# Kernel tuning notes

Measured on AMD Instinct MI355X. Metric: run time of the kernel, lower is better.

Reference implementation:

```python
import jax, jax.numpy as jnp
import numpy as np

D_MODEL = 768
NUM_HEADS = 12
DEPTH = D_MODEL // NUM_HEADS


def setup_inputs() -> dict:
    key = jax.random.key(0)
    ks = jax.random.split(key, 11)
    B, S = 2, 2048
    s = 1.0 / np.sqrt(D_MODEL)
    inp = {
        "Q": jax.random.normal(ks[0], (B, S, D_MODEL), jnp.float32),
        "K": jax.random.normal(ks[1], (B, S, D_MODEL), jnp.float32),
        "V": jax.random.normal(ks[2], (B, S, D_MODEL), jnp.float32),
        "Wq": jax.random.normal(ks[3], (D_MODEL, D_MODEL), jnp.float32) * s,
        "bq": jnp.zeros((D_MODEL,), jnp.float32),
        "Wk": jax.random.normal(ks[4], (D_MODEL, D_MODEL), jnp.float32) * s,
        "bk": jnp.zeros((D_MODEL,), jnp.float32),
        "Wv": jax.random.normal(ks[5], (D_MODEL, D_MODEL), jnp.float32) * s,
        "bv": jnp.zeros((D_MODEL,), jnp.float32),
        "Wo": jax.random.normal(ks[6], (D_MODEL, D_MODEL), jnp.float32) * s,
        "bo": jnp.zeros((D_MODEL,), jnp.float32),
    }
    return inp


def _split_heads(x):
    B, S, _ = x.shape
    return x.reshape(B, S, NUM_HEADS, DEPTH).transpose(0, 2, 1, 3)  # [B,H,S,d]


def reference(Q, K, V, Wq, bq, Wk, bk, Wv, bv, Wo, bo):
    q = _split_heads(Q @ Wq.T + bq)  # [B,H,S,d]
    k = _split_heads(K @ Wk.T + bk)
    v = _split_heads(V @ Wv.T + bv)
    scale = 1.0 / jnp.sqrt(jnp.asarray(DEPTH, q.dtype))
    scores = jnp.einsum('bhqd,bhkd->bhqk', q, k) * scale  # [B,H,S,S]
    weights = jax.nn.softmax(scores, axis=-1)
    attn = jnp.einsum('bhqk,bhkd->bhqd', weights, v)  # [B,H,S,d]
    B, H, S, d = attn.shape
    attn = attn.transpose(0, 2, 1, 3).reshape(B, S, H * d)
    out = attn @ Wo.T + bo
    return (out, weights)
```

## Files before the change

### kernel.cpp

```cpp
#include <hip/hip_runtime.h>
#include <hip/hip_bf16.h>

typedef __attribute__((ext_vector_type(4)))  float f32x4;
typedef __attribute__((ext_vector_type(16))) float f32x16;
typedef __attribute__((ext_vector_type(8)))  short s16x8;

#define MFMA(a,b,c)   __builtin_amdgcn_mfma_f32_16x16x32_bf16(a,b,c,0,0,0)
#define MFMA32(a,b,c) __builtin_amdgcn_mfma_f32_32x32x16_bf16(a,b,c,0,0,0)

__device__ __forceinline__ void gll16(const void* gptr, void* lptr){
  auto g = (const __attribute__((address_space(1))) unsigned int*)gptr;
  auto l = (__attribute__((address_space(3))) unsigned int*)lptr;
  __builtin_amdgcn_global_load_lds(g, l, 16, 0, 0);
}

__device__ __forceinline__ void split2(float x, __hip_bfloat16& h, __hip_bfloat16& l){
  h = __float2bfloat16(x);
  l = __float2bfloat16(x - __bfloat162float(h));
}

__device__ __forceinline__ unsigned short bf16bits(float x){
  __hip_bfloat16 h = __float2bfloat16(x);
  return *reinterpret_cast<unsigned short*>(&h);
}
__device__ __forceinline__ unsigned pack2(float lo, float hi){
  return (unsigned)bf16bits(lo) | ((unsigned)bf16bits(hi) << 16);
}
__device__ __forceinline__ void plane32swap(unsigned &a, unsigned &b){
  asm volatile("v_permlane32_swap_b32 %0, %1" : "+v"(a), "+v"(b));
}

__global__ __launch_bounds__(256) void split_all(
  const float* __restrict__ Q, const float* __restrict__ K, const float* __restrict__ V,
  const float* __restrict__ Wq, const float* __restrict__ Wk,
  const float* __restrict__ Wv, const float* __restrict__ Wo,
  __hip_bfloat16* __restrict__ QIh,
  __hip_bfloat16* __restrict__ KIh,
  __hip_bfloat16* __restrict__ VIh,
  __hip_bfloat16* __restrict__ Wqh,
  __hip_bfloat16* __restrict__ Wkh,
  __hip_bfloat16* __restrict__ Wvh,
  __hip_bfloat16* __restrict__ Woh, __hip_bfloat16* __restrict__ Wol)
{
  const int NE4 = 786432, WE4 = 147456;
  int i = blockIdx.x*256 + threadIdx.x;
  const float* src; __hip_bfloat16 *dh, *dl = nullptr; int off;
  if (i < 3*NE4){
    int seg = i / NE4; off = i - seg*NE4;
    src = seg==0 ? Q   : (seg==1 ? K   : V);
    dh  = seg==0 ? QIh : (seg==1 ? KIh : VIh);
  } else {
    int j = i - 3*NE4; int seg = j / WE4; off = j - seg*WE4;
    src = seg==0 ? Wq  : (seg==1 ? Wk  : (seg==2 ? Wv  : Wo));
    dh  = seg==0 ? Wqh : (seg==1 ? Wkh : (seg==2 ? Wvh : Woh));
    if (seg == 3) dl = Wol;
  }
  float4 x = ((const float4*)src)[off];
  __hip_bfloat16 h0,l0,h1,l1,h2,l2,h3,l3;
  split2(x.x,h0,l0); split2(x.y,h1,l1); split2(x.z,h2,l2); split2(x.w,h3,l3);
  union { __hip_bfloat16 b[4]; ushort4 u; } H, L;
  H.b[0]=h0; H.b[1]=h1; H.b[2]=h2; H.b[3]=h3;
  L.b[0]=l0; L.b[1]=l1; L.b[2]=l2; L.b[3]=l3;
  *(ushort4*)(dh + (size_t)off*4) = H.u;
  if (dl) *(ushort4*)(dl + (size_t)off*4) = L.u;
}

__global__ __launch_bounds__(256) void gemm_qkv(
    const __hip_bfloat16* __restrict__ QAh,
    const __hip_bfloat16* __restrict__ KAh,
    const __hip_bfloat16* __restrict__ VAh,
    const __hip_bfloat16* __restrict__ WqH,
    const __hip_bfloat16* __restrict__ WkH,
    const __hip_bfloat16* __restrict__ WvH,
    const float* __restrict__ bq, const float* __restrict__ bk, const float* __restrict__ bv,
    float qscale,
    __hip_bfloat16* __restrict__ qhp, __hip_bfloat16* __restrict__ qlp,
    __hip_bfloat16* __restrict__ khp, __hip_bfloat16* __restrict__ vTp)
{
  __shared__ __align__(16) __hip_bfloat16 lds[16384];

  const int tid = threadIdx.x;
  const int w = tid >> 6, lane = tid & 63, r = lane & 15, g = lane >> 4;
  const int wg = blockIdx.x;
  const int seg = wg / 768;
  const int t = wg % 768;
  const int tm = t / 12, tn = t % 12;

  const __hip_bfloat16* Ah = seg==0 ? QAh : (seg==1 ? KAh : VAh);
  const __hip_bfloat16* Bh = seg==0 ? WqH : (seg==1 ? WkH : WvH);
  const float* bias        = seg==0 ? bq  : (seg==1 ? bk  : bv);

  const char* gA_h = (const char*)Ah + (size_t)tm*64*768*2;
  const char* gB_h = (const char*)Bh + (size_t)tn*64*768*2;

  f32x4 acc[4] = {};

  auto stage = [&](int buf, int kbe){
    #pragma unroll
    for (int i = 0; i < 2; ++i){
      int lb = i*4096 + tid*16;
      int row = lb >> 7, colb = lb & 127;
      gll16(gA_h + (size_t)row*1536 + kbe*2 + colb, (char*)lds + buf*16384 + i*4096 + w*1024);
      gll16(gB_h + (size_t)row*1536 + kbe*2 + colb, (char*)lds + buf*16384 + 8192 + i*4096 + w*1024);
    }
  };
  int cur = 0;
  stage(0, 0);
  __syncthreads();
  for (int it = 0; it < 12; ++it){
    if (it + 1 < 12) stage(cur ^ 1, (it+1)*64);
    const __hip_bfloat16* A = lds + cur*8192;
    const __hip_bfloat16* B = lds + cur*8192 + 4096;
    #pragma unroll
    for (int c = 0; c < 2; ++c){
      int aoff = (w*16 + r)*64 + c*32 + g*8;
      s16x8 a_h = *(const s16x8*)(A + aoff);
      #pragma unroll
      for (int j = 0; j < 4; ++j){
        s16x8 b_h = *(const s16x8*)(B + (j*16 + r)*64 + c*32 + g*8);
        acc[j] = MFMA(a_h, b_h, acc[j]);
      }
    }
    __syncthreads();
    cur ^= 1;
  }

  #pragma unroll
  for (int j = 0; j < 4; ++j){
    #pragma unroll
    for (int e = 0; e < 4; ++e){
      int m = tm*64 + w*16 + g*4 + e;
      int n = tn*64 + j*16 + r;
      float v = acc[j][e] + bias[n];
      int b = m >> 11, s = m & 2047;
      if (seg == 0){
        v *= qscale;
        __hip_bfloat16 h, l; split2(v, h, l);
        size_t idx = ((size_t)(b*12 + (n>>6))*2048 + s)*64 + (n & 63);
        qhp[idx] = h; qlp[idx] = l;
      } else if (seg == 1){
        size_t idx = ((size_t)(b*12 + (n>>6))*2048 + s)*64 + (n & 63);
        khp[idx] = __float2bfloat16(v);
      } else {
        size_t idx = ((size_t)(b*12 + (n>>6))*64 + (n & 63))*2048 + s;
        vTp[idx] = __float2bfloat16(v);
      }
    }
  }
}

__global__ __launch_bounds__(256) void gemm_o(
    const __hip_bfloat16* __restrict__ Ah, const __hip_bfloat16* __restrict__ Al,
    const __hip_bfloat16* __restrict__ Bh, const __hip_bfloat16* __restrict__ Bl,
    const float* __restrict__ bias, float* __restrict__ o_f)
{
  __shared__ __align__(16) __hip_bfloat16 sAh[64*64];
  __shared__ __align__(16) __hip_bfloat16 sAl[64*64];
  __shared__ __align__(16) __hip_bfloat16 sBh[64*64];
  __shared__ __align__(16) __hip_bfloat16 sBl[64*64];

  const int tid = threadIdx.x;
  const int w = tid >> 6, lane = tid & 63, r = lane & 15, g = lane >> 4;
  const int t = blockIdx.x;
  const int tm = t / 12, tn = t % 12;

  const char* gA_h = (const char*)Ah + (size_t)tm*64*768*2;
  const char* gA_l = (const char*)Al + (size_t)tm*64*768*2;
  const char* gB_h = (const char*)Bh + (size_t)tn*64*768*2;
  const char* gB_l = (const char*)Bl + (size_t)tn*64*768*2;

  f32x4 acc[4] = {};

  for (int kb = 0; kb < 768; kb += 64){
    __syncthreads();
    #pragma unroll
    for (int i = 0; i < 2; ++i){
      int lb = i*4096 + tid*16;
      int row = lb >> 7, colb = lb & 127;
      gll16(gA_h + (size_t)row*1536 + kb*2 + colb, (char*)sAh + i*4096 + w*1024);
      gll16(gA_l + (size_t)row*1536 + kb*2 + colb, (char*)sAl + i*4096 + w*1024);
      gll16(gB_h + (size_t)row*1536 + kb*2 + colb, (char*)sBh + i*4096 + w*1024);
      gll16(gB_l + (size_t)row*1536 + kb*2 + colb, (char*)sBl + i*4096 + w*1024);
    }
    __syncthreads();
    #pragma unroll
    for (int c = 0; c < 2; ++c){
      int aoff = (w*16 + r)*64 + c*32 + g*8;
      s16x8 a_h = *(const s16x8*)(sAh + aoff);
      s16x8 a_l = *(const s16x8*)(sAl + aoff);
      #pragma unroll
      for (int j = 0; j < 4; ++j){
        int boff = (j*16 + r)*64 + c*32 + g*8;
        s16x8 b_h = *(const s16x8*)(sBh + boff);
        s16x8 b_l = *(const s16x8*)(sBl + boff);
        acc[j] = MFMA(a_h, b_h, acc[j]);
        acc[j] = MFMA(a_l, b_h, acc[j]);
        acc[j] = MFMA(a_h, b_l, acc[j]);
      }
    }
  }

  #pragma unroll
  for (int j = 0; j < 4; ++j){
    #pragma unroll
    for (int e = 0; e < 4; ++e){
      int m = tm*64 + w*16 + g*4 + e;
      int n = tn*64 + j*16 + r;
      o_f[(size_t)m*768 + n] = acc[j][e] + bias[n];
    }
  }
}

__global__ __launch_bounds__(256,4) void attn_l(
    const __hip_bfloat16* __restrict__ qh,
    const __hip_bfloat16* __restrict__ kh,
    float* __restrict__ rlbuf)
{
  __shared__ float ldsL[128];
  const int tid  = threadIdx.x;
  const int w    = tid >> 6;
  const int lane = tid & 63;
  const int col  = lane & 31;
  const int hi   = lane >> 5;
  const int bh = blockIdx.x % 24, qt = blockIdx.x / 24;

  const __hip_bfloat16* qr_h = qh + ((size_t)bh*2048 + qt*32 + col)*64 + hi*8;
  s16x8 Qh[4];
  #pragma unroll
  for (int ks = 0; ks < 4; ++ks) Qh[ks] = *(const s16x8*)(qr_h + ks*16);

  const __hip_bfloat16* kb = kh + (size_t)bh*2048*64;

  s16x8 kfn[4];
  {
    const __hip_bfloat16* kr = kb + ((size_t)(w*16)*32 + col)*64 + hi*8;
    #pragma unroll
    for (int ks = 0; ks < 4; ++ks) kfn[ks] = *(const s16x8*)(kr + ks*16);
  }

  float ps0=0.f, ps1=0.f, ps2=0.f, ps3=0.f;
  for (int c = 0; c < 16; ++c){
    s16x8 kf[4];
    #pragma unroll
    for (int ks = 0; ks < 4; ++ks) kf[ks] = kfn[ks];
    if (c < 15){
      const __hip_bfloat16* kr = kb + ((size_t)(w*16 + c + 1)*32 + col)*64 + hi*8;
      #pragma unroll
      for (int ks = 0; ks < 4; ++ks) kfn[ks] = *(const s16x8*)(kr + ks*16);
    }
    f32x16 s0;
    #pragma unroll
    for (int e = 0; e < 16; ++e) s0[e] = 0.f;
    #pragma unroll
    for (int ks = 0; ks < 4; ++ks) s0 = MFMA32(kf[ks], Qh[ks], s0);
    #pragma unroll
    for (int e = 0; e < 16; e += 4){
      ps0 += exp2f(s0[e+0]); ps1 += exp2f(s0[e+1]);
      ps2 += exp2f(s0[e+2]); ps3 += exp2f(s0[e+3]);
    }
  }
  float l_w = (ps0+ps1) + (ps2+ps3);
  l_w += __shfl_xor(l_w, 32);
  if (lane < 32) ldsL[w*32 + col] = l_w;
  __syncthreads();
  if (tid < 32){
    float lt = (ldsL[tid] + ldsL[32+tid]) + (ldsL[64+tid] + ldsL[96+tid]);
    rlbuf[(size_t)bh*2048 + qt*32 + tid] = 1.0f / lt;
  }
}

__global__ __launch_bounds__(256,4) void attn_pv(
    const __hip_bfloat16* __restrict__ qh, const __hip_bfloat16* __restrict__ ql,
    const __hip_bfloat16* __restrict__ kh,
    const __hip_bfloat16* __restrict__ vT,
    const float* __restrict__ rlbuf,
    float* __restrict__ wout,
    __hip_bfloat16* __restrict__ attnh, __hip_bfloat16* __restrict__ attnl)
{
  __shared__ __align__(16) float ldsX[4*32*36];
  __shared__ float ldsRL[32];

  const int tid  = threadIdx.x;
  const int w    = tid >> 6;
  const int lane = tid & 63;
  const int col  = lane & 31;
  const int hi   = lane >> 5;
  const int bh = blockIdx.x % 24, qt = blockIdx.x / 24;

  const __hip_bfloat16* qr_h = qh + ((size_t)bh*2048 + qt*32 + col)*64 + hi*8;
  const __hip_bfloat16* qr_l = ql + ((size_t)bh*2048 + qt*32 + col)*64 + hi*8;
  s16x8 Qh[4], Ql[4];
  #pragma unroll
  for (int ks = 0; ks < 4; ++ks){
    Qh[ks] = *(const s16x8*)(qr_h + ks*16);
    Ql[ks] = *(const s16x8*)(qr_l + ks*16);
  }

  if (tid < 32) ldsRL[tid] = rlbuf[(size_t)bh*2048 + qt*32 + tid];
  __syncthreads();
  const float rl = ldsRL[col];

  const __hip_bfloat16* kb = kh + (size_t)bh*2048*64;
  const __hip_bfloat16* vb = vT + (size_t)bh*64*2048;
  float* W = ldsX + w*1152;

  s16x8 kfn[4];
  {
    const __hip_bfloat16* kr = kb + ((size_t)(w*16)*32 + col)*64 + hi*8;
    #pragma unroll
    for (int ks = 0; ks < 4; ++ks) kfn[ks] = *(const s16x8*)(kr + ks*16);
  }

  f32x16 pv0, pv1;
  #pragma unroll
  for (int e = 0; e < 16; ++e){ pv0[e]=0.f; pv1[e]=0.f; }
  float* wq = wout + ((size_t)bh*2048 + (size_t)qt*32)*2048;

  for (int c = 0; c < 16; ++c){
    const int key0 = (w*16 + c)*32;
    s16x8 kf[4];
    #pragma unroll
    for (int ks = 0; ks < 4; ++ks) kf[ks] = kfn[ks];
    if (c < 15){
      const __hip_bfloat16* kr = kb + ((size_t)(w*16 + c + 1)*32 + col)*64 + hi*8;
      #pragma unroll
      for (int ks = 0; ks < 4; ++ks) kfn[ks] = *(const s16x8*)(kr + ks*16);
    }
    s16x8 vv[2][2];
    #pragma unroll
    for (int ww = 0; ww < 2; ++ww)
      #pragma unroll
      for (int dt = 0; dt < 2; ++dt)
        vv[ww][dt] = *(const s16x8*)(vb + ((size_t)(dt*32+col)*2048 + key0 + ww*16 + hi*8));

    f32x16 s0;
    #pragma unroll
    for (int e = 0; e < 16; ++e) s0[e] = 0.f;
    #pragma unroll
    for (int ks = 0; ks < 4; ++ks){
      s0 = MFMA32(kf[ks], Qh[ks], s0);
      s0 = MFMA32(kf[ks], Ql[ks], s0);
    }
    #pragma unroll
    for (int e = 0; e < 16; ++e) s0[e] = exp2f(s0[e]);

    #pragma unroll
    for (int rq = 0; rq < 4; ++rq){
      f32x4 f;
      f[0]=s0[rq*4+0]*rl; f[1]=s0[rq*4+1]*rl; f[2]=s0[rq*4+2]*rl; f[3]=s0[rq*4+3]*rl;
      *(f32x4*)(W + col*36 + rq*8 + hi*4) = f;
    }
    #pragma unroll
    for (int it = 0; it < 4; ++it){
      int q  = it*8 + (lane>>3);
      int k4 = (lane&7)*4;
      f32x4 f = *(const f32x4*)(W + q*36 + k4);
      *(f32x4*)(wq + (size_t)q*2048 + key0 + k4) = f;
    }

    #pragma unroll
    for (int ww = 0; ww < 2; ++ww){
      const int e0 = ww*8;
      unsigned wa = pack2(s0[e0+0], s0[e0+1]);
      unsigned wb = pack2(s0[e0+2], s0[e0+3]);
      unsigned wc = pack2(s0[e0+4], s0[e0+5]);
      unsigned wd = pack2(s0[e0+6], s0[e0+7]);
      plane32swap(wa, wc);
      plane32swap(wb, wd);
      union { unsigned u[4]; s16x8 v; } cv;
      cv.u[0]=wa; cv.u[1]=wb; cv.u[2]=wc; cv.u[3]=wd;
      pv0 = MFMA32(cv.v, vv[ww][0], pv0);
      pv1 = MFMA32(cv.v, vv[ww][1], pv1);
    }
  }

  __syncthreads();

  float* ldsPV = ldsX;
  if (w >= 2){
    const int buf = w - 2;
    #pragma unroll
    for (int e = 0; e < 16; ++e){
      ldsPV[(e)   *128 + buf*64 + lane] = pv0[e];
      ldsPV[(16+e)*128 + buf*64 + lane] = pv1[e];
    }
  }
  __syncthreads();
  if (w < 2){
    #pragma unroll
    for (int e = 0; e < 16; ++e){
      pv0[e] += ldsPV[(e)   *128 + w*64 + lane];
      pv1[e] += ldsPV[(16+e)*128 + w*64 + lane];
    }
  }
  __syncthreads();
  if (w == 1){
    #pragma unroll
    for (int e = 0; e < 16; ++e){
      ldsPV[(e)   *128 + lane] = pv0[e];
      ldsPV[(16+e)*128 + lane] = pv1[e];
    }
  }
  __syncthreads();
  if (w == 0){
    #pragma unroll
    for (int e = 0; e < 16; ++e){
      pv0[e] += ldsPV[(e)   *128 + lane];
      pv1[e] += ldsPV[(16+e)*128 + lane];
    }
    const int b_ = bh / 12, hh = bh % 12;
    #pragma unroll
    for (int e = 0; e < 16; ++e){
      int qsub = (e&3) + 8*(e>>2) + 4*hi;
      float re = ldsRL[qsub];
      int qrow = qt*32 + qsub;
      size_t base = ((size_t)b_*2048 + qrow)*768 + hh*64;
      __hip_bfloat16 h0, l0, h1, l1;
      split2(pv0[e]*re, h0, l0);
      split2(pv1[e]*re, h1, l1);
      attnh[base + col]      = h0; attnl[base + col]      = l0;
      attnh[base + 32 + col] = h1; attnl[base + 32 + col] = l1;
    }
  }
}

extern "C" void kernel_launch(void* const* d_in, const int* in_sizes, int n_in,
                              void* d_out, int out_size, void* d_ws, size_t ws_size,
                              hipStream_t stream){
  const float* Q  = (const float*)d_in[0];
  const float* Kx = (const float*)d_in[1];
  const float* V  = (const float*)d_in[2];
  const float* Wq = (const float*)d_in[3];
  const float* bq = (const float*)d_in[4];
  const float* Wk = (const float*)d_in[5];
  const float* bk = (const float*)d_in[6];
  const float* Wv = (const float*)d_in[7];
  const float* bv = (const float*)d_in[8];
  const float* Wo = (const float*)d_in[9];
  const float* bo = (const float*)d_in[10];

  float* out = (float*)d_out;
  float* wts = out + (size_t)2*2048*768;

  char* cur = (char*)d_ws;
  auto alloc = [&](size_t elems)->__hip_bfloat16*{
    __hip_bfloat16* p = (__hip_bfloat16*)cur;
    cur += ((elems*2 + 255) & ~(size_t)255);
    return p;
  };
  const size_t NE = (size_t)4096*768;
  const size_t WE = (size_t)768*768;

  __hip_bfloat16 *QIh=alloc(NE), *KIh=alloc(NE), *VIh=alloc(NE);
  __hip_bfloat16 *Wqh=alloc(WE), *Wkh=alloc(WE), *Wvh=alloc(WE),
                 *Woh=alloc(WE), *Wol=alloc(WE);
  __hip_bfloat16 *qhp=alloc(NE), *qlp=alloc(NE), *khp=alloc(NE),
                 *vTp=alloc(NE);
  __hip_bfloat16 *ath=alloc(NE), *atl=alloc(NE);
  float* rlbuf = (float*)alloc(2*24*2048);

  split_all<<<11520, 256, 0, stream>>>(Q, Kx, V, Wq, Wk, Wv, Wo,
      QIh, KIh, VIh, Wqh, Wkh, Wvh, Woh, Wol);

  gemm_qkv<<<2304, 256, 0, stream>>>(
      QIh, KIh, VIh,
      Wqh, Wkh, Wvh,
      bq, bk, bv, 0.18033688011112042f,
      qhp, qlp, khp, vTp);

  attn_l <<<1536, 256, 0, stream>>>(qhp, khp, rlbuf);
  attn_pv<<<1536, 256, 0, stream>>>(qhp, qlp, khp, vTp, rlbuf, wts, ath, atl);

  gemm_o<<<768, 256, 0, stream>>>(ath,atl,Woh,Wol,bo, out);
}
```

Baseline: 273.1 us.

## Process two query tiles per attn_l block and prioritize MFMA waves

The row-sum kernel now handles 64 queries per block instead of 32, so each K fragment loaded is reused for two MFMA chains, which halves K loads and the grid size. Both attention kernels wrap their MFMA sections in s_setprio to raise wave priority during matrix work. In attn_pv the weights store through LDS to global is moved after the PV MFMAs, so the write traffic can overlap with later work. The cost is more registers in attn_l and fewer blocks to spread across CUs.

```diff
diff --git a/kernel.cpp b/kernel.cpp
--- a/kernel.cpp
+++ b/kernel.cpp
@@ -216,18 +216,22 @@
     const __hip_bfloat16* __restrict__ kh,
     float* __restrict__ rlbuf)
 {
-  __shared__ float ldsL[128];
+  __shared__ float ldsL[2][128];
   const int tid  = threadIdx.x;
   const int w    = tid >> 6;
   const int lane = tid & 63;
   const int col  = lane & 31;
   const int hi   = lane >> 5;
-  const int bh = blockIdx.x % 24, qt = blockIdx.x / 24;
-
-  const __hip_bfloat16* qr_h = qh + ((size_t)bh*2048 + qt*32 + col)*64 + hi*8;
-  s16x8 Qh[4];
+  const int bh = blockIdx.x % 24, qt2 = blockIdx.x / 24;
+
+  const __hip_bfloat16* qr0 = qh + ((size_t)bh*2048 + qt2*64 + col)*64 + hi*8;
+  const __hip_bfloat16* qr1 = qr0 + 32*64;
+  s16x8 Qh0[4], Qh1[4];
   #pragma unroll
-  for (int ks = 0; ks < 4; ++ks) Qh[ks] = *(const s16x8*)(qr_h + ks*16);
+  for (int ks = 0; ks < 4; ++ks){
+    Qh0[ks] = *(const s16x8*)(qr0 + ks*16);
+    Qh1[ks] = *(const s16x8*)(qr1 + ks*16);
+  }
 
   const __hip_bfloat16* kb = kh + (size_t)bh*2048*64;
 
@@ -238,7 +242,8 @@
     for (int ks = 0; ks < 4; ++ks) kfn[ks] = *(const s16x8*)(kr + ks*16);
   }
 
-  float ps0=0.f, ps1=0.f, ps2=0.f, ps3=0.f;
+  float pa0=0.f, pa1=0.f, pa2=0.f, pa3=0.f;
+  float pb0=0.f, pb1=0.f, pb2=0.f, pb3=0.f;
   for (int c = 0; c < 16; ++c){
     s16x8 kf[4];
     #pragma unroll
@@ -248,24 +253,37 @@
       #pragma unroll
       for (int ks = 0; ks < 4; ++ks) kfn[ks] = *(const s16x8*)(kr + ks*16);
     }
-    f32x16 s0;
-    #pragma unroll
-    for (int e = 0; e < 16; ++e) s0[e] = 0.f;
-    #pragma unroll
-    for (int ks = 0; ks < 4; ++ks) s0 = MFMA32(kf[ks], Qh[ks], s0);
+    f32x16 s0, s1;
+    #pragma unroll
+    for (int e = 0; e < 16; ++e){ s0[e] = 0.f; s1[e] = 0.f; }
+    __builtin_amdgcn_s_setprio(1);
+    #pragma unroll
+    for (int ks = 0; ks < 4; ++ks){
+      s0 = MFMA32(kf[ks], Qh0[ks], s0);
+      s1 = MFMA32(kf[ks], Qh1[ks], s1);
+    }
+    __builtin_amdgcn_s_setprio(0);
     #pragma unroll
     for (int e = 0; e < 16; e += 4){
-      ps0 += exp2f(s0[e+0]); ps1 += exp2f(s0[e+1]);
-      ps2 += exp2f(s0[e+2]); ps3 += exp2f(s0[e+3]);
-    }
-  }
-  float l_w = (ps0+ps1) + (ps2+ps3);
-  l_w += __shfl_xor(l_w, 32);
-  if (lane < 32) ldsL[w*32 + col] = l_w;
-  __syncthreads();
-  if (tid < 32){
-    float lt = (ldsL[tid] + ldsL[32+tid]) + (ldsL[64+tid] + ldsL[96+tid]);
-    rlbuf[(size_t)bh*2048 + qt*32 + tid] = 1.0f / lt;
+      pa0 += exp2f(s0[e+0]); pa1 += exp2f(s0[e+1]);
+      pa2 += exp2f(s0[e+2]); pa3 += exp2f(s0[e+3]);
+      pb0 += exp2f(s1[e+0]); pb1 += exp2f(s1[e+1]);
+      pb2 += exp2f(s1[e+2]); pb3 += exp2f(s1[e+3]);
+    }
+  }
+  float l0 = (pa0+pa1) + (pa2+pa3);
+  float l1 = (pb0+pb1) + (pb2+pb3);
+  l0 += __shfl_xor(l0, 32);
+  l1 += __shfl_xor(l1, 32);
+  if (lane < 32){
+    ldsL[0][w*32 + col] = l0;
+    ldsL[1][w*32 + col] = l1;
+  }
+  __syncthreads();
+  if (tid < 64){
+    int tt = tid >> 5, q = tid & 31;
+    float lt = (ldsL[tt][q] + ldsL[tt][32+q]) + (ldsL[tt][64+q] + ldsL[tt][96+q]);
+    rlbuf[(size_t)bh*2048 + qt2*64 + tt*32 + q] = 1.0f / lt;
   }
 }
 
@@ -336,28 +354,17 @@
     f32x16 s0;
     #pragma unroll
     for (int e = 0; e < 16; ++e) s0[e] = 0.f;
+    __builtin_amdgcn_s_setprio(1);
     #pragma unroll
     for (int ks = 0; ks < 4; ++ks){
       s0 = MFMA32(kf[ks], Qh[ks], s0);
       s0 = MFMA32(kf[ks], Ql[ks], s0);
     }
+    __builtin_amdgcn_s_setprio(0);
     #pragma unroll
     for (int e = 0; e < 16; ++e) s0[e] = exp2f(s0[e]);
 
-    #pragma unroll
-    for (int rq = 0; rq < 4; ++rq){
-      f32x4 f;
-      f[0]=s0[rq*4+0]*rl; f[1]=s0[rq*4+1]*rl; f[2]=s0[rq*4+2]*rl; f[3]=s0[rq*4+3]*rl;
-      *(f32x4*)(W + col*36 + rq*8 + hi*4) = f;
-    }
-    #pragma unroll
-    for (int it = 0; it < 4; ++it){
-      int q  = it*8 + (lane>>3);
-      int k4 = (lane&7)*4;
-      f32x4 f = *(const f32x4*)(W + q*36 + k4);
-      *(f32x4*)(wq + (size_t)q*2048 + key0 + k4) = f;
-    }
-
+    __builtin_amdgcn_s_setprio(1);
     #pragma unroll
     for (int ww = 0; ww < 2; ++ww){
       const int e0 = ww*8;
@@ -371,6 +378,21 @@
       cv.u[0]=wa; cv.u[1]=wb; cv.u[2]=wc; cv.u[3]=wd;
       pv0 = MFMA32(cv.v, vv[ww][0], pv0);
       pv1 = MFMA32(cv.v, vv[ww][1], pv1);
+    }
+    __builtin_amdgcn_s_setprio(0);
+
+    #pragma unroll
+    for (int rq = 0; rq < 4; ++rq){
+      f32x4 f;
+      f[0]=s0[rq*4+0]*rl; f[1]=s0[rq*4+1]*rl; f[2]=s0[rq*4+2]*rl; f[3]=s0[rq*4+3]*rl;
+      *(f32x4*)(W + col*36 + rq*8 + hi*4) = f;
+    }
+    #pragma unroll
+    for (int it = 0; it < 4; ++it){
+      int q  = it*8 + (lane>>3);
+      int k4 = (lane&7)*4;
+      f32x4 f = *(const f32x4*)(W + q*36 + k4);
+      *(f32x4*)(wq + (size_t)q*2048 + key0 + k4) = f;
     }
   }
 
@@ -468,7 +490,7 @@
       bq, bk, bv, 0.18033688011112042f,
       qhp, qlp, khp, vTp);
 
-  attn_l <<<1536, 256, 0, stream>>>(qhp, khp, rlbuf);
+  attn_l <<<768,  256, 0, stream>>>(qhp, khp, rlbuf);
   attn_pv<<<1536, 256, 0, stream>>>(qhp, qlp, khp, vTp, rlbuf, wts, ath, atl);
 
   gemm_o<<<768, 256, 0, stream>>>(ath,atl,Woh,Wol,bo, out);
```

Result: slower. 331.3 us (+21.3%).
